# Optimization experiments

Hardware: AMD Instinct MI355X
Metric: run time of the kernel (lower is better)

Reference implementation:

```python
import jax, jax.numpy as jnp
import numpy as np

B, L, D, H = 2, 1024, 512, 8
h = D // H            # head_dim = 64
K = H                 # num_eigh must equal num_heads (vmap pairing in conv)
EPS = 1e-5


def _spectral_filters(seq_len: int, k: int) -> np.ndarray:
    # Hankel matrix Z_{ij} = 2 / ((i+j)^3 - (i+j)), top-k eigenvectors scaled by sigma^{1/4}
    e = np.arange(1, seq_len + 1, dtype=np.float64)
    ipj = e[:, None] + e[None, :]
    Z = 2.0 / (ipj ** 3 - ipj)
    sigma, phi = np.linalg.eigh(Z)
    sigma_k = np.clip(sigma[-k:], 1e-9, None)
    return (phi[:, -k:] * sigma_k ** 0.25).astype(np.float32)  # [L, K]


def setup_inputs() -> dict:
    key = jax.random.key(0)
    ks = jax.random.split(key, 8)
    s = 0.02
    return {
        "x": jax.random.normal(ks[0], (B, L, D), jnp.float32),
        "spectral_basis": jnp.asarray(_spectral_filters(L, K)),       # [L, K]
        "wq_w": jax.random.normal(ks[1], (D, D), jnp.float32) * s,
        "wq_b": jnp.zeros((D,), jnp.float32),
        "wk_w": jax.random.normal(ks[2], (D, D), jnp.float32) * s,
        "wk_b": jnp.zeros((D,), jnp.float32),
        "wv_w": jax.random.normal(ks[3], (D, D), jnp.float32) * s,
        "wv_b": jnp.zeros((D,), jnp.float32),
        "wo_w": jax.random.normal(ks[4], (D, D), jnp.float32) * s,
        "wo_b": jnp.zeros((D,), jnp.float32),
        "wg_w": jax.random.normal(ks[5], (h * h,), jnp.float32) * s,  # Linear(h^2 -> 1)
        "wg_b": jnp.zeros((), jnp.float32),
    }


def _causal_fft_conv(u, filt_f, n):
    # u: [B,H,L,h]; filt_f: precomputed rfft of per-head filters [H, F]
    Uf = jnp.fft.rfft(u, n=n, axis=2)                        # [B,H,F,h]
    y = jnp.fft.irfft(Uf * filt_f[None, :, :, None], n=n, axis=2)
    return y[:, :, :L]                                       # truncate full conv -> causal


def reference(x, spectral_basis, wq_w, wq_b, wk_w, wk_b, wv_w, wv_b,
              wo_w, wo_b, wg_w, wg_b):
    # projections -> [B,H,L,h]
    q = (x @ wq_w + wq_b).reshape(B, L, H, h).transpose(0, 2, 1, 3)
    k = (x @ wk_w + wk_b).reshape(B, L, H, h).transpose(0, 2, 1, 3) * h ** (-0.5)
    v = (x @ wv_w + wv_b).reshape(B, L, H, h).transpose(0, 2, 1, 3)

    n = 2 * L
    filt_f = jnp.fft.rfft(spectral_basis.T, n=n, axis=1)     # [H, F] (one filter per head)
    k_conv = _causal_fft_conv(k, filt_f, n)
    v_conv = _causal_fft_conv(v, filt_f, n)

    # gated outer product Z: [B,H,L,h,h]
    Z = jnp.einsum('bhlm,bhln->bhlmn', v_conv, k_conv)
    gate_logits = Z.reshape(B, H, L, h * h) @ wg_w + wg_b    # [B,H,L]
    gates = jax.nn.relu(gate_logits) ** 2 + EPS
    gated_Z = gates[..., None, None] * Z

    # associative scan (additive) over sequence dim
    cumul_gated_Z = jnp.cumsum(gated_Z, axis=2)              # [B,H,L,h,h]
    cumul_gates = jnp.cumsum(gates, axis=2)                  # [B,H,L]
    attn = cumul_gated_Z / (cumul_gates[..., None, None] + EPS)

    # note: original einsum sums over l (and d) independently of s
    ctxt = jnp.einsum('bhsd,bhlde->bhse', q, attn)           # [B,H,L,h]
    norm = jnp.linalg.norm(ctxt, axis=3, keepdims=True)
    unit = ctxt / jnp.maximum(norm, EPS)                     # F.normalize semantics
    out = unit.transpose(0, 2, 1, 3).reshape(B, L, D)
    return out @ wo_w + wo_b
```

## Files before the change

### kernel.cpp

```cpp
#include <hip/hip_runtime.h>
#include <math.h>


typedef __attribute__((ext_vector_type(8))) short short8;
typedef __attribute__((ext_vector_type(4))) float floatx4;

__device__ __forceinline__ unsigned short f2bf(float f) {
    unsigned int u = __float_as_uint(f);
    unsigned int r = (u + 0x7FFFu + ((u >> 16) & 1u)) >> 16;
    return (unsigned short)r;
}

__global__ __launch_bounds__(256) void k_prep(
    const float* __restrict__ x,
    const float* __restrict__ wq, const float* __restrict__ wk,
    const float* __restrict__ wv, const float* __restrict__ wo,
    const float* __restrict__ wg,
    unsigned short* __restrict__ xb,
    unsigned short* __restrict__ wT, unsigned short* __restrict__ woT,
    unsigned short* __restrict__ wgb)
{
    __shared__ float sf[64][65];
    const int blk = blockIdx.x;
    const int tid = threadIdx.x;

    if (blk < 512) {
        const int gid = blk * 256 + tid;
        const float4* x4 = (const float4*)x;
        float4 a = x4[gid*2], b = x4[gid*2+1];
        uint4 o;
        o.x = f2bf(a.x) | ((unsigned)f2bf(a.y) << 16);
        o.y = f2bf(a.z) | ((unsigned)f2bf(a.w) << 16);
        o.z = f2bf(b.x) | ((unsigned)f2bf(b.y) << 16);
        o.w = f2bf(b.z) | ((unsigned)f2bf(b.w) << 16);
        ((uint4*)xb)[gid] = o;
    } else if (blk < 768) {
        const int t = blk - 512;
        const float* src; unsigned short* dst; int n0, c0, k0;
        if (t < 192) {
            int nt = t >> 3, kt = t & 7;
            n0 = nt * 64; k0 = kt * 64;
            int z = n0 >> 9; c0 = n0 & 511;
            src = (z == 0) ? wq : (z == 1) ? wk : wv;
            dst = wT;
        } else {
            int u = t - 192; int nt = u >> 3, kt = u & 7;
            n0 = nt * 64; c0 = n0; k0 = kt * 64;
            src = wo; dst = woT;
        }
        const int rr = tid >> 4, c4 = tid & 15;
        #pragma unroll
        for (int g = 0; g < 4; ++g) {
            int r = g*16 + rr;
            float4 v = *(const float4*)&src[(size_t)(k0 + r)*512 + c0 + c4*4];
            sf[r][c4*4+0]=v.x; sf[r][c4*4+1]=v.y; sf[r][c4*4+2]=v.z; sf[r][c4*4+3]=v.w;
        }
        __syncthreads();
        #pragma unroll
        for (int g = 0; g < 4; ++g) {
            int c = g*16 + rr;
            int kk = c4*4;
            ushort4 o;
            o.x = f2bf(sf[kk+0][c]); o.y = f2bf(sf[kk+1][c]);
            o.z = f2bf(sf[kk+2][c]); o.w = f2bf(sf[kk+3][c]);
            *(ushort4*)&dst[(size_t)(n0 + c)*512 + k0 + kk] = o;
        }
    } else {
        const float4* wg4 = (const float4*)wg;
        for (int i = tid; i < 512; i += 256) {
            float4 a = wg4[i*2], b = wg4[i*2+1];
            uint4 o;
            o.x = f2bf(a.x) | ((unsigned)f2bf(a.y) << 16);
            o.y = f2bf(a.z) | ((unsigned)f2bf(a.w) << 16);
            o.z = f2bf(b.x) | ((unsigned)f2bf(b.y) << 16);
            o.w = f2bf(b.z) | ((unsigned)f2bf(b.w) << 16);
            ((uint4*)wgb)[i] = o;
        }
    }
}

__global__ __launch_bounds__(256) void k_qkv_mfma(
    const unsigned short* __restrict__ xb, const unsigned short* __restrict__ wT,
    const float* __restrict__ bq, const float* __restrict__ bk,
    const float* __restrict__ bv,
    float* __restrict__ qo, unsigned short* __restrict__ ub2)
{
    const int tid = threadIdx.x;
    const int lane = tid & 63, wave = tid >> 6;
    const int q = lane >> 4, ln = lane & 15;
    const int wm = wave * 32;
    const int m0 = blockIdx.y * 128;
    const int n0 = blockIdx.x * 64;

    __shared__ unsigned short As[128*72];
    __shared__ unsigned short Bs[64*72];

    floatx4 acc[2][4];
    #pragma unroll
    for (int i = 0; i < 2; ++i)
        #pragma unroll
        for (int j = 0; j < 4; ++j)
            acc[i][j] = (floatx4){0.f, 0.f, 0.f, 0.f};

    const uint4* Ag = (const uint4*)xb;
    const uint4* Bg = (const uint4*)wT;
    for (int k0 = 0; k0 < 512; k0 += 64) {
        #pragma unroll
        for (int s = 0; s < 4; ++s) {
            int idx = s*256 + tid;
            int r = idx >> 3, cp = idx & 7;
            uint4 va = Ag[(size_t)(m0 + r)*64 + (k0 >> 3) + cp];
            *(uint4*)&As[r*72 + cp*8] = va;
        }
        #pragma unroll
        for (int s = 0; s < 2; ++s) {
            int idx = s*256 + tid;
            int r = idx >> 3, cp = idx & 7;
            uint4 vb = Bg[(size_t)(n0 + r)*64 + (k0 >> 3) + cp];
            *(uint4*)&Bs[r*72 + cp*8] = vb;
        }
        __syncthreads();
        short8 af0[2], af1[2], bf0[4], bf1[4];
        #pragma unroll
        for (int i = 0; i < 2; ++i) {
            af0[i] = *(const short8*)&As[(wm + i*16 + ln)*72 + q*8];
            af1[i] = *(const short8*)&As[(wm + i*16 + ln)*72 + 32 + q*8];
        }
        #pragma unroll
        for (int i = 0; i < 4; ++i) {
            bf0[i] = *(const short8*)&Bs[(i*16 + ln)*72 + q*8];
            bf1[i] = *(const short8*)&Bs[(i*16 + ln)*72 + 32 + q*8];
        }
        #pragma unroll
        for (int mi = 0; mi < 2; ++mi)
            #pragma unroll
            for (int ni = 0; ni < 4; ++ni) {
                acc[mi][ni] = __builtin_amdgcn_mfma_f32_16x16x32_bf16(
                    af0[mi], bf0[ni], acc[mi][ni], 0, 0, 0);
                acc[mi][ni] = __builtin_amdgcn_mfma_f32_16x16x32_bf16(
                    af1[mi], bf1[ni], acc[mi][ni], 0, 0, 0);
            }
        __syncthreads();
    }

    const int z = n0 >> 9;
    if (z == 0) {
        #pragma unroll
        for (int mi = 0; mi < 2; ++mi) {
            #pragma unroll
            for (int ni = 0; ni < 4; ++ni) {
                int c = (n0 + ni*16 + ln) & 511;
                int head = c >> 6, dd = c & 63;
                float bb = bq[c];
                #pragma unroll
                for (int reg = 0; reg < 4; ++reg) {
                    int row = m0 + wm + mi*16 + q*4 + reg;
                    int b = row >> 10, l = row & 1023;
                    qo[(size_t)((b*8 + head)*1024 + l)*64 + dd] =
                        acc[mi][ni][reg] + bb;
                }
            }
        }
    } else {
        const float scale = (z == 1) ? 0.125f : 1.0f;
        const float* bias = (z == 1) ? bk : bv;
        unsigned short* dst = ub2 + (size_t)(z-1) * 16 * 64 * 1024;
        #pragma unroll
        for (int mi = 0; mi < 2; ++mi) {
            #pragma unroll
            for (int ni = 0; ni < 4; ++ni) {
                int c = (n0 + ni*16 + ln) & 511;
                int head = c >> 6, dd = c & 63;
                float bb = bias[c];
                int row0 = m0 + wm + mi*16 + q*4;
                int b = row0 >> 10, l0 = row0 & 1023;
                ushort4 o;
                o.x = f2bf((acc[mi][ni][0] + bb) * scale);
                o.y = f2bf((acc[mi][ni][1] + bb) * scale);
                o.z = f2bf((acc[mi][ni][2] + bb) * scale);
                o.w = f2bf((acc[mi][ni][3] + bb) * scale);
                *(ushort4*)&dst[((size_t)((b*8 + head)*64) + dd)*1024 + l0] = o;
            }
        }
    }
}

__global__ __launch_bounds__(256) void k_conv_gate(
    const float* __restrict__ sb,
    const unsigned short* __restrict__ ub2,
    const unsigned short* __restrict__ wgb, const float* __restrict__ wg_b,
    float* __restrict__ kc, float* __restrict__ vc,
    float* __restrict__ gl)
{
    const int tid = threadIdx.x;
    const int lane = tid & 63, wave = tid >> 6;
    const int q = lane >> 4, ln = lane & 15;
    const int bh  = blockIdx.x, h = bh & 7;
    const int it  = blockIdx.y;
    const int t0  = it * 64;

    __shared__ unsigned short revf[1152];
    __shared__ unsigned short Bk[64*72];
    __shared__ unsigned short Bv[64*72];

    for (int i = tid; i < 1152; i += 256) {
        int d = 1087 - i;
        revf[i] = (d >= 0 && d < 1024) ? f2bf(sb[d*8 + h]) : (unsigned short)0;
    }

    const uint4* Bg = (const uint4*)ub2;
    const size_t bk_base = (size_t)bh * 8192;
    const size_t bv_base = (size_t)(16 + bh) * 8192;

    floatx4 acck[4], accv[4];
    #pragma unroll
    for (int i = 0; i < 4; ++i) {
        acck[i] = (floatx4){0.f,0.f,0.f,0.f};
        accv[i] = (floatx4){0.f,0.f,0.f,0.f};
    }

    const int kend = t0 + 64;
    const int arow = 1087 - t0 - (wave*16 + ln);
    for (int k0 = 0; k0 < kend; k0 += 64) {
        #pragma unroll
        for (int s = 0; s < 2; ++s) {
            int idx = s*256 + tid;
            int r = idx >> 3, cp = idx & 7;
            *(uint4*)&Bk[r*72 + cp*8] = Bg[bk_base + (size_t)r*128 + (k0 >> 3) + cp];
            *(uint4*)&Bv[r*72 + cp*8] = Bg[bv_base + (size_t)r*128 + (k0 >> 3) + cp];
        }
        __syncthreads();
        const int ab = arow + k0 + q*8;
        short8 a0, a1;
        #pragma unroll
        for (int j = 0; j < 8; ++j) {
            a0[j] = (short)revf[ab + j];
            a1[j] = (short)revf[ab + 32 + j];
        }
        #pragma unroll
        for (int ni = 0; ni < 4; ++ni) {
            short8 kb0 = *(const short8*)&Bk[(ni*16 + ln)*72 + q*8];
            short8 kb1 = *(const short8*)&Bk[(ni*16 + ln)*72 + 32 + q*8];
            short8 vb0 = *(const short8*)&Bv[(ni*16 + ln)*72 + q*8];
            short8 vb1 = *(const short8*)&Bv[(ni*16 + ln)*72 + 32 + q*8];
            acck[ni] = __builtin_amdgcn_mfma_f32_16x16x32_bf16(a0, kb0, acck[ni], 0, 0, 0);
            acck[ni] = __builtin_amdgcn_mfma_f32_16x16x32_bf16(a1, kb1, acck[ni], 0, 0, 0);
            accv[ni] = __builtin_amdgcn_mfma_f32_16x16x32_bf16(a0, vb0, accv[ni], 0, 0, 0);
            accv[ni] = __builtin_amdgcn_mfma_f32_16x16x32_bf16(a1, vb1, accv[ni], 0, 0, 0);
        }
        __syncthreads();
    }

    float* kdst = kc + (size_t)bh * 65536;
    float* vdst = vc + (size_t)bh * 65536;
    #pragma unroll
    for (int ni = 0; ni < 4; ++ni)
        #pragma unroll
        for (int reg = 0; reg < 4; ++reg) {
            int row = wave*16 + q*4 + reg;
            int grow = t0 + row;
            kdst[(size_t)grow*64 + ni*16 + ln] = acck[ni][reg];
            vdst[(size_t)grow*64 + ni*16 + ln] = accv[ni][reg];
            Bk[row*72 + ni*16 + ln] = f2bf(acck[ni][reg]);
        }
    {
        const uint4* Wg = (const uint4*)wgb;
        #pragma unroll
        for (int s = 0; s < 2; ++s) {
            int idx = s*256 + tid;
            int r = idx >> 3, cp = idx & 7;
            *(uint4*)&Bv[r*72 + cp*8] = Wg[r*8 + cp];
        }
    }
    __syncthreads();

    floatx4 T[4];
    #pragma unroll
    for (int mt = 0; mt < 4; ++mt) T[mt] = (floatx4){0.f,0.f,0.f,0.f};
    #pragma unroll
    for (int k0g = 0; k0g < 64; k0g += 32) {
        short8 a = *(const short8*)&Bk[(wave*16 + ln)*72 + k0g + q*8];
        #pragma unroll
        for (int mt = 0; mt < 4; ++mt) {
            short8 b = *(const short8*)&Bv[(mt*16 + ln)*72 + k0g + q*8];
            T[mt] = __builtin_amdgcn_mfma_f32_16x16x32_bf16(a, b, T[mt], 0, 0, 0);
        }
    }

    float part[4] = {0.f, 0.f, 0.f, 0.f};
    #pragma unroll
    for (int mt = 0; mt < 4; ++mt)
        #pragma unroll
        for (int reg = 0; reg < 4; ++reg)
            part[reg] += T[mt][reg] * accv[mt][reg];
    #pragma unroll
    for (int reg = 0; reg < 4; ++reg) {
        part[reg] += __shfl_xor(part[reg], 1);
        part[reg] += __shfl_xor(part[reg], 2);
        part[reg] += __shfl_xor(part[reg], 4);
        part[reg] += __shfl_xor(part[reg], 8);
    }
    if (ln == 0) {
        const float wgbias = wg_b[0];
        #pragma unroll
        for (int reg = 0; reg < 4; ++reg) {
            int l = t0 + wave*16 + q*4 + reg;
            float s = part[reg] + wgbias;
            float rr = fmaxf(s, 0.0f);
            gl[bh*1024 + l] = rr*rr + 1e-5f;
        }
    }
}

__global__ __launch_bounds__(256) void k_amat(
    const float* __restrict__ kc, const float* __restrict__ vc,
    const float* __restrict__ gl, float* __restrict__ apart)
{
    const int tid = threadIdx.x, tx = tid & 15, ty = tid >> 4;
    const int lane = tid & 63, wave = tid >> 6;
    const int bh = blockIdx.x, slc = blockIdx.y;
    const float* kb = kc + (size_t)bh * 65536;
    const float* vb = vc + (size_t)bh * 65536;

    __shared__ float scanA[4], scanB[4];
    __shared__ float wfull[1024];
    __shared__ __align__(16) float vs[16][68];
    __shared__ __align__(16) float ks2[16][68];

    {
        const float4 g4 = ((const float4*)(gl + bh*1024))[tid];
        float g[4] = {g4.x, g4.y, g4.z, g4.w};
        float p[4];
        p[0]=g[0]; p[1]=p[0]+g[1]; p[2]=p[1]+g[2]; p[3]=p[2]+g[3];
        float x = p[3];
        #pragma unroll
        for (int off = 1; off < 64; off <<= 1) {
            float t = __shfl_up(x, off);
            if (lane >= off) x += t;
        }
        if (lane == 63) scanA[wave] = x;
        __syncthreads();
        float wb = 0.f;
        #pragma unroll
        for (int wv = 0; wv < 4; ++wv) wb += (wv < wave) ? scanA[wv] : 0.f;
        const float base = wb + x - p[3];
        float r[4], pr[4];
        #pragma unroll
        for (int u = 0; u < 4; ++u) r[u] = 1.0f / (base + p[u] + 1e-5f);
        pr[0]=r[0]; pr[1]=pr[0]+r[1]; pr[2]=pr[1]+r[2]; pr[3]=pr[2]+r[3];
        float y = pr[3];
        #pragma unroll
        for (int off = 1; off < 64; off <<= 1) {
            float t = __shfl_up(y, off);
            if (lane >= off) y += t;
        }
        if (lane == 63) scanB[wave] = y;
        __syncthreads();
        float rb = 0.f, Rtot = 0.f;
        #pragma unroll
        for (int wv = 0; wv < 4; ++wv) {
            rb   += (wv < wave) ? scanB[wv] : 0.f;
            Rtot += scanB[wv];
        }
        const float baser = rb + y - pr[3];
        wfull[tid*4+0] = g[0] * (Rtot - (baser + pr[0] - pr[3]) - pr[3] + pr[3] - (pr[0] - r[0]) - r[0] + r[0]);
        wfull[tid*4+0] = g[0] * (Rtot - (baser + pr[0]) + r[0]);
        wfull[tid*4+1] = g[1] * (Rtot - (baser + pr[1]) + r[1]);
        wfull[tid*4+2] = g[2] * (Rtot - (baser + pr[2]) + r[2]);
        wfull[tid*4+3] = g[3] * (Rtot - (baser + pr[3]) + r[3]);
    }
    __syncthreads();

    float acc[4][4] = {};
    const float4* k4 = (const float4*)kb;
    const float4* v4 = (const float4*)vb;
    for (int j0 = slc*64; j0 < slc*64 + 64; j0 += 16) {
        {
            int r = tid >> 4, c4 = tid & 15;
            *(float4*)&vs[r][c4*4]  = v4[(size_t)(j0 + r)*16 + c4];
            *(float4*)&ks2[r][c4*4] = k4[(size_t)(j0 + r)*16 + c4];
        }
        __syncthreads();
        #pragma unroll
        for (int jj = 0; jj < 16; ++jj) {
            float wj = wfull[j0 + jj];
            float a[4];
            a[0] = vs[jj][ty*4+0]*wj; a[1] = vs[jj][ty*4+1]*wj;
            a[2] = vs[jj][ty*4+2]*wj; a[3] = vs[jj][ty*4+3]*wj;
            float4 b4 = *(const float4*)&ks2[jj][tx*4];
            float bb[4] = {b4.x, b4.y, b4.z, b4.w};
            #pragma unroll
            for (int ii = 0; ii < 4; ++ii)
                #pragma unroll
                for (int jc = 0; jc < 4; ++jc)
                    acc[ii][jc] += a[ii] * bb[jc];
        }
        __syncthreads();
    }
    float* ap = apart + (size_t)(slc*16 + bh) * 4096;
    #pragma unroll
    for (int i = 0; i < 4; ++i) {
        float4 o = { acc[i][0], acc[i][1], acc[i][2], acc[i][3] };
        *(float4*)&ap[(ty*4+i)*64 + tx*4] = o;
    }
}

__global__ __launch_bounds__(256) void k_ctxt(
    const float* __restrict__ q, const float* __restrict__ apart,
    unsigned short* __restrict__ ub)
{
    const int tid = threadIdx.x, tx = tid & 15, ty = tid >> 4;
    const int l0 = blockIdx.x * 64;
    const int bh = blockIdx.y;
    const float* qb = q + (size_t)bh * 65536;

    __shared__ __align__(16) float qs[64][20];
    __shared__ __align__(16) float As[16][68];
    float acc[4][4] = {};
    const float4* q4 = (const float4*)qb;
    const float4* a4 = (const float4*)apart;
    for (int d0 = 0; d0 < 64; d0 += 16) {
        {
            int r = tid >> 2, c4 = tid & 3;
            float4 t = q4[(size_t)(l0 + r)*16 + (d0 >> 2) + c4];
            *(float4*)&qs[r][c4*4] = t;
        }
        {
            int r = tid >> 4, c4 = tid & 15;
            size_t o = (size_t)(d0 + r)*16 + c4;
            float4 t = a4[(size_t)(0*16 + bh)*1024 + o];
            #pragma unroll
            for (int s = 1; s < 16; ++s) {
                float4 u = a4[(size_t)(s*16 + bh)*1024 + o];
                t.x += u.x; t.y += u.y; t.z += u.z; t.w += u.w;
            }
            *(float4*)&As[r][c4*4] = t;
        }
        __syncthreads();
        float qreg[4][16];
        #pragma unroll
        for (int i = 0; i < 4; ++i)
            #pragma unroll
            for (int c = 0; c < 4; ++c) {
                float4 t = *(const float4*)&qs[ty*4+i][c*4];
                qreg[i][c*4+0] = t.x; qreg[i][c*4+1] = t.y;
                qreg[i][c*4+2] = t.z; qreg[i][c*4+3] = t.w;
            }
        #pragma unroll
        for (int dd = 0; dd < 16; ++dd) {
            float4 b4 = *(const float4*)&As[dd][tx*4];
            float bb[4] = {b4.x, b4.y, b4.z, b4.w};
            #pragma unroll
            for (int ii = 0; ii < 4; ++ii)
                #pragma unroll
                for (int jj = 0; jj < 4; ++jj)
                    acc[ii][jj] += qreg[ii][dd] * bb[jj];
        }
        __syncthreads();
    }
    __shared__ float red[64][17];
    __shared__ float nrm[64];
    #pragma unroll
    for (int i = 0; i < 4; ++i) {
        red[ty*4+i][tx] = acc[i][0]*acc[i][0] + acc[i][1]*acc[i][1]
                        + acc[i][2]*acc[i][2] + acc[i][3]*acc[i][3];
    }
    __syncthreads();
    if (tid < 64) {
        float s = 0.0f;
        #pragma unroll
        for (int t = 0; t < 16; ++t) s += red[tid][t];
        nrm[tid] = fmaxf(sqrtf(s), 1e-5f);
    }
    __syncthreads();
    const int b = bh >> 3, hd = bh & 7;
    #pragma unroll
    for (int i = 0; i < 4; ++i) {
        int lr = ty*4 + i;
        float inv = 1.0f / nrm[lr];
        ushort4 o;
        o.x = f2bf(acc[i][0]*inv); o.y = f2bf(acc[i][1]*inv);
        o.z = f2bf(acc[i][2]*inv); o.w = f2bf(acc[i][3]*inv);
        *(ushort4*)&ub[(size_t)(b*1024 + l0 + lr)*512 + hd*64 + tx*4] = o;
    }
}

__global__ __launch_bounds__(256) void k_out_mfma(
    const unsigned short* __restrict__ ub, const unsigned short* __restrict__ woT,
    const float* __restrict__ bo, float* __restrict__ out)
{
    const int tid = threadIdx.x;
    const int lane = tid & 63, wave = tid >> 6;
    const int q = lane >> 4, ln = lane & 15;
    const int wm = wave * 32;
    const int m0 = blockIdx.y * 128;
    const int n0 = blockIdx.x * 64;

    __shared__ unsigned short As[128*72];
    __shared__ unsigned short Bs[64*72];

    floatx4 acc[2][4];
    #pragma unroll
    for (int i = 0; i < 2; ++i)
        #pragma unroll
        for (int j = 0; j < 4; ++j)
            acc[i][j] = (floatx4){0.f, 0.f, 0.f, 0.f};

    const uint4* Ag = (const uint4*)ub;
    const uint4* Bg = (const uint4*)woT;
    for (int k0 = 0; k0 < 512; k0 += 64) {
        #pragma unroll
        for (int s = 0; s < 4; ++s) {
            int idx = s*256 + tid;
            int r = idx >> 3, cp = idx & 7;
            uint4 va = Ag[(size_t)(m0 + r)*64 + (k0 >> 3) + cp];
            *(uint4*)&As[r*72 + cp*8] = va;
        }
        #pragma unroll
        for (int s = 0; s < 2; ++s) {
            int idx = s*256 + tid;
            int r = idx >> 3, cp = idx & 7;
            uint4 vb = Bg[(size_t)(n0 + r)*64 + (k0 >> 3) + cp];
            *(uint4*)&Bs[r*72 + cp*8] = vb;
        }
        __syncthreads();
        short8 af0[2], af1[2], bf0[4], bf1[4];
        #pragma unroll
        for (int i = 0; i < 2; ++i) {
            af0[i] = *(const short8*)&As[(wm + i*16 + ln)*72 + q*8];
            af1[i] = *(const short8*)&As[(wm + i*16 + ln)*72 + 32 + q*8];
        }
        #pragma unroll
        for (int i = 0; i < 4; ++i) {
            bf0[i] = *(const short8*)&Bs[(i*16 + ln)*72 + q*8];
            bf1[i] = *(const short8*)&Bs[(i*16 + ln)*72 + 32 + q*8];
        }
        #pragma unroll
        for (int mi = 0; mi < 2; ++mi)
            #pragma unroll
            for (int ni = 0; ni < 4; ++ni) {
                acc[mi][ni] = __builtin_amdgcn_mfma_f32_16x16x32_bf16(
                    af0[mi], bf0[ni], acc[mi][ni], 0, 0, 0);
                acc[mi][ni] = __builtin_amdgcn_mfma_f32_16x16x32_bf16(
                    af1[mi], bf1[ni], acc[mi][ni], 0, 0, 0);
            }
        __syncthreads();
    }

    #pragma unroll
    for (int mi = 0; mi < 2; ++mi) {
        #pragma unroll
        for (int ni = 0; ni < 4; ++ni) {
            int gcol = n0 + ni*16 + ln;
            float bb = bo[gcol];
            #pragma unroll
            for (int reg = 0; reg < 4; ++reg) {
                int row = m0 + wm + mi*16 + q*4 + reg;
                out[(size_t)row*512 + gcol] = acc[mi][ni][reg] + bb;
            }
        }
    }
}

extern "C" void kernel_launch(void* const* d_in, const int* in_sizes, int n_in,
                              void* d_out, int out_size, void* d_ws, size_t ws_size,
                              hipStream_t stream)
{
    const float* x   = (const float*)d_in[0];
    const float* sb  = (const float*)d_in[1];
    const float* wq  = (const float*)d_in[2];
    const float* bq  = (const float*)d_in[3];
    const float* wk  = (const float*)d_in[4];
    const float* bk  = (const float*)d_in[5];
    const float* wv  = (const float*)d_in[6];
    const float* bv  = (const float*)d_in[7];
    const float* wo  = (const float*)d_in[8];
    const float* bo  = (const float*)d_in[9];
    const float* wg  = (const float*)d_in[10];
    const float* wgb = (const float*)d_in[11];
    float* out = (float*)d_out;
    float* ws  = (float*)d_ws;

    float* Q   = ws;
    float* KC  = ws + 1048576;
    float* VC  = ws + 2*1048576;
    float* GL  = ws + 3*1048576;
    float* AP  = GL + 16384;
    float* fp  = AP + 1048576;
    unsigned short* XB  = (unsigned short*)fp;
    unsigned short* WT  = XB  + 1048576;
    unsigned short* WOT = WT  + 786432;
    unsigned short* UB  = WOT + 262144;
    unsigned short* UB2 = UB  + 1048576;
    unsigned short* WGB = UB2 + 2097152;

    k_prep     <<<dim3(769),    256, 0, stream>>>(x, wq, wk, wv, wo, wg,
                                                  XB, WT, WOT, WGB);
    k_qkv_mfma <<<dim3(24, 16), 256, 0, stream>>>(XB, WT, bq, bk, bv, Q, UB2);
    k_conv_gate<<<dim3(16, 16), 256, 0, stream>>>(sb, UB2, WGB, wgb, KC, VC, GL);
    k_amat     <<<dim3(16, 16), 256, 0, stream>>>(KC, VC, GL, AP);
    k_ctxt     <<<dim3(16, 16), 256, 0, stream>>>(Q, AP, UB);
    k_out_mfma <<<dim3(8, 16),  256, 0, stream>>>(UB, WOT, bo, out);
}
```

Before: 143.7 us.

## Fuse bf16 conversion prep into QKV GEMM and retile output projection

Removes the separate prep kernel. Fp32 x and the QKV weights are now converted to bf16 while being staged into shared memory inside the QKV GEMM, and the gate weights are converted inside the conv kernel. The wo transpose/convert runs in the first 64 QKV blocks. The QKV GEMM tile grows to 256 rows, and the output GEMM uses smaller 64x64 tiles to launch more blocks. This saves one launch and the bf16 intermediate round trips. In exchange it repeats the conversion work per block and reads the weights with strided scalar loads.

```diff
diff --git a/kernel.cpp b/kernel.cpp
--- a/kernel.cpp
+++ b/kernel.cpp
@@ -11,48 +11,37 @@
     return (unsigned short)r;
 }
 
-__global__ __launch_bounds__(256) void k_prep(
+__global__ __launch_bounds__(256) void k_qkv(
     const float* __restrict__ x,
     const float* __restrict__ wq, const float* __restrict__ wk,
     const float* __restrict__ wv, const float* __restrict__ wo,
-    const float* __restrict__ wg,
-    unsigned short* __restrict__ xb,
-    unsigned short* __restrict__ wT, unsigned short* __restrict__ woT,
-    unsigned short* __restrict__ wgb)
+    const float* __restrict__ bq, const float* __restrict__ bk,
+    const float* __restrict__ bv,
+    unsigned short* __restrict__ WOT,
+    float* __restrict__ Qb, unsigned short* __restrict__ UB2)
 {
-    __shared__ float sf[64][65];
-    const int blk = blockIdx.x;
     const int tid = threadIdx.x;
-
-    if (blk < 512) {
-        const int gid = blk * 256 + tid;
-        const float4* x4 = (const float4*)x;
-        float4 a = x4[gid*2], b = x4[gid*2+1];
-        uint4 o;
-        o.x = f2bf(a.x) | ((unsigned)f2bf(a.y) << 16);
-        o.y = f2bf(a.z) | ((unsigned)f2bf(a.w) << 16);
-        o.z = f2bf(b.x) | ((unsigned)f2bf(b.y) << 16);
-        o.w = f2bf(b.z) | ((unsigned)f2bf(b.w) << 16);
-        ((uint4*)xb)[gid] = o;
-    } else if (blk < 768) {
-        const int t = blk - 512;
-        const float* src; unsigned short* dst; int n0, c0, k0;
-        if (t < 192) {
-            int nt = t >> 3, kt = t & 7;
-            n0 = nt * 64; k0 = kt * 64;
-            int z = n0 >> 9; c0 = n0 & 511;
-            src = (z == 0) ? wq : (z == 1) ? wk : wv;
-            dst = wT;
-        } else {
-            int u = t - 192; int nt = u >> 3, kt = u & 7;
-            n0 = nt * 64; c0 = n0; k0 = kt * 64;
-            src = wo; dst = woT;
-        }
+    const int lane = tid & 63, wave = tid >> 6;
+    const int qd = lane >> 4, ln = lane & 15;
+    const int nt = blockIdx.x, mg = blockIdx.y;
+    const int n0 = nt * 64;
+    const int z = n0 >> 9, c0 = n0 & 511;
+    const float* wsrc = (z == 0) ? wq : (z == 1) ? wk : wv;
+
+    __shared__ __align__(16) unsigned char arena[46080];
+    unsigned short* As = (unsigned short*)arena;
+    unsigned short* Bs = (unsigned short*)(arena + 36864);
+
+    const int flat = mg * 24 + nt;
+    if (flat < 64) {
+        float (*sf)[65] = (float(*)[65])arena;
+        const int nt2 = flat >> 3, kt = flat & 7;
+        const int n0p = nt2 * 64, k0p = kt * 64;
         const int rr = tid >> 4, c4 = tid & 15;
         #pragma unroll
         for (int g = 0; g < 4; ++g) {
             int r = g*16 + rr;
-            float4 v = *(const float4*)&src[(size_t)(k0 + r)*512 + c0 + c4*4];
+            float4 v = *(const float4*)&wo[(size_t)(k0p + r)*512 + n0p + c4*4];
             sf[r][c4*4+0]=v.x; sf[r][c4*4+1]=v.y; sf[r][c4*4+2]=v.z; sf[r][c4*4+3]=v.w;
         }
         __syncthreads();
@@ -63,76 +52,67 @@
             ushort4 o;
             o.x = f2bf(sf[kk+0][c]); o.y = f2bf(sf[kk+1][c]);
             o.z = f2bf(sf[kk+2][c]); o.w = f2bf(sf[kk+3][c]);
-            *(ushort4*)&dst[(size_t)(n0 + c)*512 + k0 + kk] = o;
-        }
-    } else {
-        const float4* wg4 = (const float4*)wg;
-        for (int i = tid; i < 512; i += 256) {
-            float4 a = wg4[i*2], b = wg4[i*2+1];
+            *(ushort4*)&WOT[(size_t)(n0p + c)*512 + k0p + kk] = o;
+        }
+    }
+    __syncthreads();
+
+    const int m0 = mg * 256;
+    const int wm = wave * 64;
+
+    floatx4 acc[4][4];
+    #pragma unroll
+    for (int i = 0; i < 4; ++i)
+        #pragma unroll
+        for (int j = 0; j < 4; ++j)
+            acc[i][j] = (floatx4){0.f, 0.f, 0.f, 0.f};
+
+    for (int k0 = 0; k0 < 512; k0 += 64) {
+        #pragma unroll
+        for (int s = 0; s < 8; ++s) {
+            int idx = s*256 + tid;
+            int r = idx >> 3, cp = idx & 7;
+            const float* xs = &x[(size_t)(m0 + r)*512 + k0 + cp*8];
+            float4 a = *(const float4*)xs;
+            float4 b = *(const float4*)(xs + 4);
             uint4 o;
             o.x = f2bf(a.x) | ((unsigned)f2bf(a.y) << 16);
             o.y = f2bf(a.z) | ((unsigned)f2bf(a.w) << 16);
             o.z = f2bf(b.x) | ((unsigned)f2bf(b.y) << 16);
             o.w = f2bf(b.z) | ((unsigned)f2bf(b.w) << 16);
-            ((uint4*)wgb)[i] = o;
-        }
-    }
-}
-
-__global__ __launch_bounds__(256) void k_qkv_mfma(
-    const unsigned short* __restrict__ xb, const unsigned short* __restrict__ wT,
-    const float* __restrict__ bq, const float* __restrict__ bk,
-    const float* __restrict__ bv,
-    float* __restrict__ qo, unsigned short* __restrict__ ub2)
-{
-    const int tid = threadIdx.x;
-    const int lane = tid & 63, wave = tid >> 6;
-    const int q = lane >> 4, ln = lane & 15;
-    const int wm = wave * 32;
-    const int m0 = blockIdx.y * 128;
-    const int n0 = blockIdx.x * 64;
-
-    __shared__ unsigned short As[128*72];
-    __shared__ unsigned short Bs[64*72];
-
-    floatx4 acc[2][4];
-    #pragma unroll
-    for (int i = 0; i < 2; ++i)
-        #pragma unroll
-        for (int j = 0; j < 4; ++j)
-            acc[i][j] = (floatx4){0.f, 0.f, 0.f, 0.f};
-
-    const uint4* Ag = (const uint4*)xb;
-    const uint4* Bg = (const uint4*)wT;
-    for (int k0 = 0; k0 < 512; k0 += 64) {
-        #pragma unroll
-        for (int s = 0; s < 4; ++s) {
-            int idx = s*256 + tid;
-            int r = idx >> 3, cp = idx & 7;
-            uint4 va = Ag[(size_t)(m0 + r)*64 + (k0 >> 3) + cp];
-            *(uint4*)&As[r*72 + cp*8] = va;
-        }
-        #pragma unroll
-        for (int s = 0; s < 2; ++s) {
-            int idx = s*256 + tid;
-            int r = idx >> 3, cp = idx & 7;
-            uint4 vb = Bg[(size_t)(n0 + r)*64 + (k0 >> 3) + cp];
-            *(uint4*)&Bs[r*72 + cp*8] = vb;
-        }
-        __syncthreads();
-        short8 af0[2], af1[2], bf0[4], bf1[4];
-        #pragma unroll
-        for (int i = 0; i < 2; ++i) {
-            af0[i] = *(const short8*)&As[(wm + i*16 + ln)*72 + q*8];
-            af1[i] = *(const short8*)&As[(wm + i*16 + ln)*72 + 32 + q*8];
-        }
-        #pragma unroll
-        for (int i = 0; i < 4; ++i) {
-            bf0[i] = *(const short8*)&Bs[(i*16 + ln)*72 + q*8];
-            bf1[i] = *(const short8*)&Bs[(i*16 + ln)*72 + 32 + q*8];
-        }
-        #pragma unroll
-        for (int mi = 0; mi < 2; ++mi)
+            *(uint4*)&As[r*72 + cp*8] = o;
+        }
+        {
+            float v[16];
+            #pragma unroll
+            for (int j = 0; j < 16; ++j)
+                v[j] = wsrc[(size_t)(k0 + wave*16 + j)*512 + c0 + lane];
+            uint4 o1, o2;
+            o1.x = f2bf(v[0])  | ((unsigned)f2bf(v[1])  << 16);
+            o1.y = f2bf(v[2])  | ((unsigned)f2bf(v[3])  << 16);
+            o1.z = f2bf(v[4])  | ((unsigned)f2bf(v[5])  << 16);
+            o1.w = f2bf(v[6])  | ((unsigned)f2bf(v[7])  << 16);
+            o2.x = f2bf(v[8])  | ((unsigned)f2bf(v[9])  << 16);
+            o2.y = f2bf(v[10]) | ((unsigned)f2bf(v[11]) << 16);
+            o2.z = f2bf(v[12]) | ((unsigned)f2bf(v[13]) << 16);
+            o2.w = f2bf(v[14]) | ((unsigned)f2bf(v[15]) << 16);
+            *(uint4*)&Bs[lane*72 + wave*16]     = o1;
+            *(uint4*)&Bs[lane*72 + wave*16 + 8] = o2;
+        }
+        __syncthreads();
+        short8 af0[4], af1[4], bf0[4], bf1[4];
+        #pragma unroll
+        for (int mi = 0; mi < 4; ++mi) {
+            af0[mi] = *(const short8*)&As[(wm + mi*16 + ln)*72 + qd*8];
+            af1[mi] = *(const short8*)&As[(wm + mi*16 + ln)*72 + 32 + qd*8];
+        }
+        #pragma unroll
+        for (int ni = 0; ni < 4; ++ni) {
+            bf0[ni] = *(const short8*)&Bs[(ni*16 + ln)*72 + qd*8];
+            bf1[ni] = *(const short8*)&Bs[(ni*16 + ln)*72 + 32 + qd*8];
+        }
+        #pragma unroll
+        for (int mi = 0; mi < 4; ++mi)
             #pragma unroll
             for (int ni = 0; ni < 4; ++ni) {
                 acc[mi][ni] = __builtin_amdgcn_mfma_f32_16x16x32_bf16(
@@ -143,10 +123,9 @@
         __syncthreads();
     }
 
-    const int z = n0 >> 9;
     if (z == 0) {
         #pragma unroll
-        for (int mi = 0; mi < 2; ++mi) {
+        for (int mi = 0; mi < 4; ++mi) {
             #pragma unroll
             for (int ni = 0; ni < 4; ++ni) {
                 int c = (n0 + ni*16 + ln) & 511;
@@ -154,9 +133,9 @@
                 float bb = bq[c];
                 #pragma unroll
                 for (int reg = 0; reg < 4; ++reg) {
-                    int row = m0 + wm + mi*16 + q*4 + reg;
+                    int row = m0 + wm + mi*16 + qd*4 + reg;
                     int b = row >> 10, l = row & 1023;
-                    qo[(size_t)((b*8 + head)*1024 + l)*64 + dd] =
+                    Qb[(size_t)((b*8 + head)*1024 + l)*64 + dd] =
                         acc[mi][ni][reg] + bb;
                 }
             }
@@ -164,15 +143,15 @@
     } else {
         const float scale = (z == 1) ? 0.125f : 1.0f;
         const float* bias = (z == 1) ? bk : bv;
-        unsigned short* dst = ub2 + (size_t)(z-1) * 16 * 64 * 1024;
-        #pragma unroll
-        for (int mi = 0; mi < 2; ++mi) {
+        unsigned short* dst = UB2 + (size_t)(z-1) * 16 * 64 * 1024;
+        #pragma unroll
+        for (int mi = 0; mi < 4; ++mi) {
             #pragma unroll
             for (int ni = 0; ni < 4; ++ni) {
                 int c = (n0 + ni*16 + ln) & 511;
                 int head = c >> 6, dd = c & 63;
                 float bb = bias[c];
-                int row0 = m0 + wm + mi*16 + q*4;
+                int row0 = m0 + wm + mi*16 + qd*4;
                 int b = row0 >> 10, l0 = row0 & 1023;
                 ushort4 o;
                 o.x = f2bf((acc[mi][ni][0] + bb) * scale);
@@ -188,7 +167,7 @@
 __global__ __launch_bounds__(256) void k_conv_gate(
     const float* __restrict__ sb,
     const unsigned short* __restrict__ ub2,
-    const unsigned short* __restrict__ wgb, const float* __restrict__ wg_b,
+    const float* __restrict__ wgw, const float* __restrict__ wg_b,
     float* __restrict__ kc, float* __restrict__ vc,
     float* __restrict__ gl)
 {
@@ -263,14 +242,19 @@
             vdst[(size_t)grow*64 + ni*16 + ln] = accv[ni][reg];
             Bk[row*72 + ni*16 + ln] = f2bf(acck[ni][reg]);
         }
-    {
-        const uint4* Wg = (const uint4*)wgb;
-        #pragma unroll
-        for (int s = 0; s < 2; ++s) {
-            int idx = s*256 + tid;
-            int r = idx >> 3, cp = idx & 7;
-            *(uint4*)&Bv[r*72 + cp*8] = Wg[r*8 + cp];
-        }
+    #pragma unroll
+    for (int s = 0; s < 2; ++s) {
+        int idx = s*256 + tid;
+        int r = idx >> 3, cp = idx & 7;
+        const float* ws2 = &wgw[r*64 + cp*8];
+        float4 a = *(const float4*)ws2;
+        float4 b = *(const float4*)(ws2 + 4);
+        uint4 o;
+        o.x = f2bf(a.x) | ((unsigned)f2bf(a.y) << 16);
+        o.y = f2bf(a.z) | ((unsigned)f2bf(a.w) << 16);
+        o.z = f2bf(b.x) | ((unsigned)f2bf(b.y) << 16);
+        o.w = f2bf(b.z) | ((unsigned)f2bf(b.w) << 16);
+        *(uint4*)&Bv[r*72 + cp*8] = o;
     }
     __syncthreads();
 
@@ -363,7 +347,6 @@
             Rtot += scanB[wv];
         }
         const float baser = rb + y - pr[3];
-        wfull[tid*4+0] = g[0] * (Rtot - (baser + pr[0] - pr[3]) - pr[3] + pr[3] - (pr[0] - r[0]) - r[0] + r[0]);
         wfull[tid*4+0] = g[0] * (Rtot - (baser + pr[0]) + r[0]);
         wfull[tid*4+1] = g[1] * (Rtot - (baser + pr[1]) + r[1]);
         wfull[tid*4+2] = g[2] * (Rtot - (baser + pr[2]) + r[2]);
@@ -485,79 +468,54 @@
     }
 }
 
-__global__ __launch_bounds__(256) void k_out_mfma(
+__global__ __launch_bounds__(256) void k_out(
     const unsigned short* __restrict__ ub, const unsigned short* __restrict__ woT,
     const float* __restrict__ bo, float* __restrict__ out)
 {
     const int tid = threadIdx.x;
     const int lane = tid & 63, wave = tid >> 6;
-    const int q = lane >> 4, ln = lane & 15;
-    const int wm = wave * 32;
-    const int m0 = blockIdx.y * 128;
-    const int n0 = blockIdx.x * 64;
-
-    __shared__ unsigned short As[128*72];
+    const int qd = lane >> 4, ln = lane & 15;
+    const int m0 = (blockIdx.x >> 3) * 64;
+    const int n0 = (blockIdx.x & 7) * 64;
+
+    __shared__ unsigned short As[64*72];
     __shared__ unsigned short Bs[64*72];
 
-    floatx4 acc[2][4];
-    #pragma unroll
-    for (int i = 0; i < 2; ++i)
-        #pragma unroll
-        for (int j = 0; j < 4; ++j)
-            acc[i][j] = (floatx4){0.f, 0.f, 0.f, 0.f};
+    floatx4 acc[4];
+    #pragma unroll
+    for (int i = 0; i < 4; ++i) acc[i] = (floatx4){0.f,0.f,0.f,0.f};
 
     const uint4* Ag = (const uint4*)ub;
     const uint4* Bg = (const uint4*)woT;
     for (int k0 = 0; k0 < 512; k0 += 64) {
         #pragma unroll
-        for (int s = 0; s < 4; ++s) {
-            int idx = s*256 + tid;
-            int r = idx >> 3, cp = idx & 7;
-            uint4 va = Ag[(size_t)(m0 + r)*64 + (k0 >> 3) + cp];
-            *(uint4*)&As[r*72 + cp*8] = va;
-        }
-        #pragma unroll
         for (int s = 0; s < 2; ++s) {
             int idx = s*256 + tid;
             int r = idx >> 3, cp = idx & 7;
-            uint4 vb = Bg[(size_t)(n0 + r)*64 + (k0 >> 3) + cp];
-            *(uint4*)&Bs[r*72 + cp*8] = vb;
-        }
-        __syncthreads();
-        short8 af0[2], af1[2], bf0[4], bf1[4];
-        #pragma unroll
-        for (int i = 0; i < 2; ++i) {
-            af0[i] = *(const short8*)&As[(wm + i*16 + ln)*72 + q*8];
-            af1[i] = *(const short8*)&As[(wm + i*16 + ln)*72 + 32 + q*8];
-        }
-        #pragma unroll
-        for (int i = 0; i < 4; ++i) {
-            bf0[i] = *(const short8*)&Bs[(i*16 + ln)*72 + q*8];
-            bf1[i] = *(const short8*)&Bs[(i*16 + ln)*72 + 32 + q*8];
-        }
-        #pragma unroll
-        for (int mi = 0; mi < 2; ++mi)
-            #pragma unroll
-            for (int ni = 0; ni < 4; ++ni) {
-                acc[mi][ni] = __builtin_amdgcn_mfma_f32_16x16x32_bf16(
-                    af0[mi], bf0[ni], acc[mi][ni], 0, 0, 0);
-                acc[mi][ni] = __builtin_amdgcn_mfma_f32_16x16x32_bf16(
-                    af1[mi], bf1[ni], acc[mi][ni], 0, 0, 0);
-            }
-        __syncthreads();
-    }
-
-    #pragma unroll
-    for (int mi = 0; mi < 2; ++mi) {
+            *(uint4*)&As[r*72 + cp*8] = Ag[(size_t)(m0 + r)*64 + (k0 >> 3) + cp];
+            *(uint4*)&Bs[r*72 + cp*8] = Bg[(size_t)(n0 + r)*64 + (k0 >> 3) + cp];
+        }
+        __syncthreads();
+        short8 af0 = *(const short8*)&As[(wave*16 + ln)*72 + qd*8];
+        short8 af1 = *(const short8*)&As[(wave*16 + ln)*72 + 32 + qd*8];
         #pragma unroll
         for (int ni = 0; ni < 4; ++ni) {
-            int gcol = n0 + ni*16 + ln;
-            float bb = bo[gcol];
-            #pragma unroll
-            for (int reg = 0; reg < 4; ++reg) {
-                int row = m0 + wm + mi*16 + q*4 + reg;
-                out[(size_t)row*512 + gcol] = acc[mi][ni][reg] + bb;
-            }
+            short8 bf0 = *(const short8*)&Bs[(ni*16 + ln)*72 + qd*8];
+            short8 bf1 = *(const short8*)&Bs[(ni*16 + ln)*72 + 32 + qd*8];
+            acc[ni] = __builtin_amdgcn_mfma_f32_16x16x32_bf16(af0, bf0, acc[ni], 0, 0, 0);
+            acc[ni] = __builtin_amdgcn_mfma_f32_16x16x32_bf16(af1, bf1, acc[ni], 0, 0, 0);
+        }
+        __syncthreads();
+    }
+
+    #pragma unroll
+    for (int ni = 0; ni < 4; ++ni) {
+        int gcol = n0 + ni*16 + ln;
+        float bb = bo[gcol];
+        #pragma unroll
+        for (int reg = 0; reg < 4; ++reg) {
+            int row = m0 + wave*16 + qd*4 + reg;
+            out[(size_t)row*512 + gcol] = acc[ni][reg] + bb;
         }
     }
 }
@@ -581,24 +539,20 @@
     float* out = (float*)d_out;
     float* ws  = (float*)d_ws;
 
-    float* Q   = ws;
-    float* KC  = ws + 1048576;
-    float* VC  = ws + 2*1048576;
-    float* GL  = ws + 3*1048576;
+    float* Qb  = ws;
+    float* KC  = Qb + 1048576;
+    float* VC  = KC + 1048576;
+    float* GL  = VC + 1048576;
     float* AP  = GL + 16384;
     float* fp  = AP + 1048576;
-    unsigned short* XB  = (unsigned short*)fp;
-    unsigned short* WT  = XB  + 1048576;
-    unsigned short* WOT = WT  + 786432;
+    unsigned short* WOT = (unsigned short*)fp;
     unsigned short* UB  = WOT + 262144;
     unsigned short* UB2 = UB  + 1048576;
-    unsigned short* WGB = UB2 + 2097152;
-
-    k_prep     <<<dim3(769),    256, 0, stream>>>(x, wq, wk, wv, wo, wg,
-                                                  XB, WT, WOT, WGB);
-    k_qkv_mfma <<<dim3(24, 16), 256, 0, stream>>>(XB, WT, bq, bk, bv, Q, UB2);
-    k_conv_gate<<<dim3(16, 16), 256, 0, stream>>>(sb, UB2, WGB, wgb, KC, VC, GL);
+
+    k_qkv      <<<dim3(24, 8),  256, 0, stream>>>(x, wq, wk, wv, wo,
+                                                  bq, bk, bv, WOT, Qb, UB2);
+    k_conv_gate<<<dim3(16, 16), 256, 0, stream>>>(sb, UB2, wg, wgb, KC, VC, GL);
     k_amat     <<<dim3(16, 16), 256, 0, stream>>>(KC, VC, GL, AP);
-    k_ctxt     <<<dim3(16, 16), 256, 0, stream>>>(Q, AP, UB);
-    k_out_mfma <<<dim3(8, 16),  256, 0, stream>>>(UB, WOT, bo, out);
-}
+    k_ctxt     <<<dim3(16, 16), 256, 0, stream>>>(Qb, AP, UB);
+    k_out      <<<dim3(256),    256, 0, stream>>>(UB, WOT, bo, out);
+}
```

Measured after the change: 162.2 us. +12.9%, slower.
